# Performance work log

Measured on AMD Instinct MI355X. Metric: run time of the kernel, lower is better.

The kernel has to match this reference:

```python
import jax, jax.numpy as jnp
import numpy as np
import math

B, N, F_IN, F_OUT = 16, 2048, 256, 64


def setup_inputs() -> dict:
    key = jax.random.key(0)
    k1, k2, k3, k4 = jax.random.split(key, 4)
    x = jax.random.normal(k1, (B, N, F_IN), dtype=jnp.float32)
    adj = jax.random.randint(k2, (B, N, N), 0, 2, dtype=jnp.int32)
    stdv = 1.0 / math.sqrt(F_OUT)
    weight = jax.random.uniform(k3, (F_IN, F_OUT), dtype=jnp.float32, minval=-stdv, maxval=stdv)
    # weight2 stdv = 1/sqrt(1) = 1.0
    weight2 = jax.random.uniform(k4, (2 * F_OUT, 1), dtype=jnp.float32, minval=-1.0, maxval=1.0)
    return {"x": x, "adj": adj, "weight": weight, "weight2": weight2}


def reference(x, adj, weight, weight2):
    # h[b,n,o] = (x @ weight)  -- shared linear projection
    h = jnp.einsum("bni,io->bno", x, weight)
    Fo = weight.shape[1]
    # Split additive-attention vector: e_ij = relu(h_i . a_src + h_j . a_dst)
    # Mathematically identical to cat([h_i, h_j]) @ weight2 of the original.
    a_src = weight2[:Fo, 0]
    a_dst = weight2[Fo:, 0]
    s_src = jnp.einsum("bno,o->bn", h, a_src)  # [B, N]
    s_dst = jnp.einsum("bno,o->bn", h, a_dst)  # [B, N]
    e = jax.nn.relu(s_src[:, :, None] + s_dst[:, None, :])  # [B, N, N]
    NEG = jnp.float32(-9e15)
    scores = jnp.where(adj > 0, e, NEG)
    attention = jax.nn.softmax(scores, axis=2)  # softmax over neighbors j
    # dropout = 0.0 / eval mode -> identity
    out = jnp.einsum("bij,bjo->bio", attention, h)  # [B, N, F_OUT]
    return out
```

## Files before the change

kernel.cpp:

```cpp
#include <hip/hip_runtime.h>
#include <hip/hip_bf16.h>

#define BB 16
#define NN 2048
#define FIN 256
#define FO 64

typedef __bf16 bf16x8 __attribute__((ext_vector_type(8)));
typedef float  f32x4  __attribute__((ext_vector_type(4)));
typedef int    i32x4  __attribute__((ext_vector_type(4)));
typedef unsigned int uint;

__global__ __launch_bounds__(256) void k_pack(const int* __restrict__ adj,
                                              unsigned char* __restrict__ mask) {
    size_t t = (size_t)blockIdx.x * 256 + threadIdx.x;
    const i32x4* ap = (const i32x4*)(adj + t * 8);
    i32x4 a0 = __builtin_nontemporal_load(ap);
    i32x4 a1 = __builtin_nontemporal_load(ap + 1);
    unsigned b = (unsigned)(a0.x > 0) | ((unsigned)(a0.y > 0) << 1) |
                 ((unsigned)(a0.z > 0) << 2) | ((unsigned)(a0.w > 0) << 3) |
                 ((unsigned)(a1.x > 0) << 4) | ((unsigned)(a1.y > 0) << 5) |
                 ((unsigned)(a1.z > 0) << 6) | ((unsigned)(a1.w > 0) << 7);
    mask[t] = (unsigned char)b;
}

__global__ __launch_bounds__(256) void k1_gemm(
    const float* __restrict__ x, const float* __restrict__ weight,
    const float* __restrict__ w2,
    __bf16* __restrict__ hT, float* __restrict__ s_src, float* __restrict__ s_dst) {
    __shared__ __bf16 WtL[FO * 264];
    __shared__ float vsL[FIN], vdL[FIN];
    int t = threadIdx.x;
    {
        const float4* wr = (const float4*)(weight + t * FO);
        float a = 0.f, d = 0.f;
#pragma unroll
        for (int c = 0; c < 16; ++c) {
            float4 v = wr[c];
            int o = c * 4;
            WtL[(o + 0) * 264 + t] = (__bf16)v.x;
            WtL[(o + 1) * 264 + t] = (__bf16)v.y;
            WtL[(o + 2) * 264 + t] = (__bf16)v.z;
            WtL[(o + 3) * 264 + t] = (__bf16)v.w;
            a += v.x * w2[o] + v.y * w2[o + 1] + v.z * w2[o + 2] + v.w * w2[o + 3];
            d += v.x * w2[FO + o] + v.y * w2[FO + o + 1] +
                 v.z * w2[FO + o + 2] + v.w * w2[FO + o + 3];
        }
        vsL[t] = a;
        vdL[t] = d;
    }
    __syncthreads();

    int lane = threadIdx.x & 63, w = threadIdx.x >> 6;
    int quad = lane >> 4, m = lane & 15;
    int Rbase = blockIdx.x * 64 + w * 16;
    int R = Rbase + m;
    const float* xr = x + (long)R * FIN;

    f32x4 acc[4] = {};
    float ps = 0.f, pd = 0.f;

#pragma unroll
    for (int k0 = 0; k0 < FIN; k0 += 32) {
        int kb = k0 + quad * 8;
        float4 x0 = *(const float4*)(xr + kb);
        float4 x1 = *(const float4*)(xr + kb + 4);
        float4 u0 = *(const float4*)(vsL + kb);
        float4 u1 = *(const float4*)(vsL + kb + 4);
        float4 t0 = *(const float4*)(vdL + kb);
        float4 t1 = *(const float4*)(vdL + kb + 4);
        ps += x0.x * u0.x + x0.y * u0.y + x0.z * u0.z + x0.w * u0.w +
              x1.x * u1.x + x1.y * u1.y + x1.z * u1.z + x1.w * u1.w;
        pd += x0.x * t0.x + x0.y * t0.y + x0.z * t0.z + x0.w * t0.w +
              x1.x * t1.x + x1.y * t1.y + x1.z * t1.z + x1.w * t1.w;
        bf16x8 bf = {(__bf16)x0.x, (__bf16)x0.y, (__bf16)x0.z, (__bf16)x0.w,
                     (__bf16)x1.x, (__bf16)x1.y, (__bf16)x1.z, (__bf16)x1.w};
#pragma unroll
        for (int ot = 0; ot < 4; ++ot) {
            bf16x8 af = *(const bf16x8*)(WtL + (ot * 16 + m) * 264 + kb);
            acc[ot] = __builtin_amdgcn_mfma_f32_16x16x32_bf16(af, bf, acc[ot], 0, 0, 0);
        }
    }
    ps += __shfl_xor(ps, 16);
    ps += __shfl_xor(ps, 32);
    pd += __shfl_xor(pd, 16);
    pd += __shfl_xor(pd, 32);
    if (quad == 0) {
        s_src[R] = ps;
        s_dst[R] = pd;
    }
    int b = R >> 11;
    int nb = Rbase & (NN - 1);
#pragma unroll
    for (int ot = 0; ot < 4; ++ot) {
#pragma unroll
        for (int r = 0; r < 4; ++r) {
            int o = ot * 16 + quad * 4 + r;
            hT[((long)b * FO + o) * NN + nb + m] = (__bf16)acc[ot][r];
        }
    }
}

__global__ __launch_bounds__(64, 4) void k2_attn(
    const unsigned char* __restrict__ mask, const float* __restrict__ s_src,
    const float* __restrict__ s_dst, const __bf16* __restrict__ hT,
    float* __restrict__ out) {
    __shared__ float EL[NN];
    int b = blockIdx.x >> 7;
    int rowbase = (blockIdx.x & 127) << 4;
    int lane = threadIdx.x & 63;
    int quad = lane >> 4, m = lane & 15;
    int row = rowbase + m;

    const float* sd = s_dst + b * NN;
    float mx = -3.0e38f;
    for (int j = lane; j < NN; j += 64) mx = fmaxf(mx, sd[j]);
#pragma unroll
    for (int off = 32; off >= 1; off >>= 1) mx = fmaxf(mx, __shfl_xor(mx, off));
    for (int t = lane; t < NN; t += 64) EL[t] = __expf(sd[t] - mx);

    float T = s_src[b * NN + row] + mx;
    float cK = __expf(-T);

    const uint4* mrow = (const uint4*)(mask + ((size_t)(b * NN + row)) * 256);
    const __bf16* hTb = hT + (long)b * FO * NN;
    int q8 = quad * 8;

    f32x4 acc[4] = {};
    f32x4 accL = {};
    const bf16x8 ones = {(__bf16)1.f, (__bf16)1.f, (__bf16)1.f, (__bf16)1.f,
                         (__bf16)1.f, (__bf16)1.f, (__bf16)1.f, (__bf16)1.f};

#pragma unroll
    for (int g = 0; g < 4; ++g) {
        uint4 mv0 = mrow[g * 4 + 0];
        uint4 mv1 = mrow[g * 4 + 1];
        uint4 mv2 = mrow[g * 4 + 2];
        uint4 mv3 = mrow[g * 4 + 3];
        uint mg[16] = {mv0.x, mv0.y, mv0.z, mv0.w, mv1.x, mv1.y, mv1.z, mv1.w,
                       mv2.x, mv2.y, mv2.z, mv2.w, mv3.x, mv3.y, mv3.z, mv3.w};
#pragma unroll
        for (int u = 0; u < 16; ++u) {
            int ks = g * 16 + u;
            uint mb = (mg[u] >> q8) & 0xffu;
            const float* ep = EL + ks * 32 + q8;
            float4 e0 = *(const float4*)ep;
            float4 e1 = *(const float4*)(ep + 4);
            float p0 = (mb & 1u)   ? fmaxf(e0.x, cK) : 0.f;
            float p1 = (mb & 2u)   ? fmaxf(e0.y, cK) : 0.f;
            float p2 = (mb & 4u)   ? fmaxf(e0.z, cK) : 0.f;
            float p3 = (mb & 8u)   ? fmaxf(e0.w, cK) : 0.f;
            float p4 = (mb & 16u)  ? fmaxf(e1.x, cK) : 0.f;
            float p5 = (mb & 32u)  ? fmaxf(e1.y, cK) : 0.f;
            float p6 = (mb & 64u)  ? fmaxf(e1.z, cK) : 0.f;
            float p7 = (mb & 128u) ? fmaxf(e1.w, cK) : 0.f;
            bf16x8 af = {(__bf16)p0, (__bf16)p1, (__bf16)p2, (__bf16)p3,
                         (__bf16)p4, (__bf16)p5, (__bf16)p6, (__bf16)p7};
            accL = __builtin_amdgcn_mfma_f32_16x16x32_bf16(af, ones, accL, 0, 0, 0);
            const __bf16* hb = hTb + ks * 32 + q8;
#pragma unroll
            for (int ot = 0; ot < 4; ++ot) {
                bf16x8 bf = *(const bf16x8*)(hb + (ot * 16 + m) * NN);
                acc[ot] = __builtin_amdgcn_mfma_f32_16x16x32_bf16(af, bf, acc[ot], 0, 0, 0);
            }
        }
    }

    float* outp = out + ((long)b * NN + rowbase) * FO;
#pragma unroll
    for (int r = 0; r < 4; ++r) {
        int orow = quad * 4 + r;
        float inv = 1.0f / accL[r];
#pragma unroll
        for (int ot = 0; ot < 4; ++ot) {
            outp[(long)orow * FO + ot * 16 + m] = acc[ot][r] * inv;
        }
    }
}

extern "C" void kernel_launch(void* const* d_in, const int* in_sizes, int n_in,
                              void* d_out, int out_size, void* d_ws, size_t ws_size,
                              hipStream_t stream) {
    const float* x      = (const float*)d_in[0];
    const int*   adj    = (const int*)d_in[1];
    const float* weight = (const float*)d_in[2];
    const float* w2     = (const float*)d_in[3];
    float* out = (float*)d_out;

    char* ws = (char*)d_ws;
    __bf16* hT   = (__bf16*)ws;
    float* s_src = (float*)(ws + 4194304);
    float* s_dst = (float*)(ws + 4194304 + 131072);
    unsigned char* mask = (unsigned char*)(ws + 4194304 + 262144);

    k_pack<<<32768, 256, 0, stream>>>(adj, mask);
    k1_gemm<<<512, 256, 0, stream>>>(x, weight, w2, hT, s_src, s_dst);
    k2_attn<<<2048, 64, 0, stream>>>(mask, s_src, s_dst, hT, out);
}
```

Measured before the change: 439.1 us.

## Stage h chunks in LDS shared by four waves per attention block

```diff
diff --git a/kernel.cpp b/kernel.cpp
--- a/kernel.cpp
+++ b/kernel.cpp
@@ -5,23 +5,29 @@
 #define NN 2048
 #define FIN 256
 #define FO 64
+#define CH 256
+#define HSTR 264
 
 typedef __bf16 bf16x8 __attribute__((ext_vector_type(8)));
 typedef float  f32x4  __attribute__((ext_vector_type(4)));
 typedef int    i32x4  __attribute__((ext_vector_type(4)));
 typedef unsigned int uint;
+typedef unsigned short ushort;
 
 __global__ __launch_bounds__(256) void k_pack(const int* __restrict__ adj,
-                                              unsigned char* __restrict__ mask) {
+                                              ushort* __restrict__ mask) {
     size_t t = (size_t)blockIdx.x * 256 + threadIdx.x;
-    const i32x4* ap = (const i32x4*)(adj + t * 8);
-    i32x4 a0 = __builtin_nontemporal_load(ap);
-    i32x4 a1 = __builtin_nontemporal_load(ap + 1);
-    unsigned b = (unsigned)(a0.x > 0) | ((unsigned)(a0.y > 0) << 1) |
-                 ((unsigned)(a0.z > 0) << 2) | ((unsigned)(a0.w > 0) << 3) |
-                 ((unsigned)(a1.x > 0) << 4) | ((unsigned)(a1.y > 0) << 5) |
-                 ((unsigned)(a1.z > 0) << 6) | ((unsigned)(a1.w > 0) << 7);
-    mask[t] = (unsigned char)b;
+    const i32x4* ap = (const i32x4*)(adj + t * 16);
+    i32x4 a0 = ap[0], a1 = ap[1], a2 = ap[2], a3 = ap[3];
+    uint b = (uint)(a0.x > 0) | ((uint)(a0.y > 0) << 1) |
+             ((uint)(a0.z > 0) << 2) | ((uint)(a0.w > 0) << 3) |
+             ((uint)(a1.x > 0) << 4) | ((uint)(a1.y > 0) << 5) |
+             ((uint)(a1.z > 0) << 6) | ((uint)(a1.w > 0) << 7) |
+             ((uint)(a2.x > 0) << 8) | ((uint)(a2.y > 0) << 9) |
+             ((uint)(a2.z > 0) << 10) | ((uint)(a2.w > 0) << 11) |
+             ((uint)(a3.x > 0) << 12) | ((uint)(a3.y > 0) << 13) |
+             ((uint)(a3.z > 0) << 14) | ((uint)(a3.w > 0) << 15);
+    mask[t] = (ushort)b;
 }
 
 __global__ __launch_bounds__(256) void k1_gemm(
@@ -101,15 +107,17 @@
     }
 }
 
-__global__ __launch_bounds__(64, 4) void k2_attn(
+__global__ __launch_bounds__(256, 4) void k2_attn(
     const unsigned char* __restrict__ mask, const float* __restrict__ s_src,
     const float* __restrict__ s_dst, const __bf16* __restrict__ hT,
     float* __restrict__ out) {
+    __shared__ __bf16 hL[FO * HSTR];
     __shared__ float EL[NN];
-    int b = blockIdx.x >> 7;
-    int rowbase = (blockIdx.x & 127) << 4;
-    int lane = threadIdx.x & 63;
+    int b = blockIdx.x >> 5;
+    int i0 = (blockIdx.x & 31) << 6;
+    int lane = threadIdx.x & 63, w = threadIdx.x >> 6;
     int quad = lane >> 4, m = lane & 15;
+    int rowbase = i0 + w * 16;
     int row = rowbase + m;
 
     const float* sd = s_dst + b * NN;
@@ -117,33 +125,52 @@
     for (int j = lane; j < NN; j += 64) mx = fmaxf(mx, sd[j]);
 #pragma unroll
     for (int off = 32; off >= 1; off >>= 1) mx = fmaxf(mx, __shfl_xor(mx, off));
-    for (int t = lane; t < NN; t += 64) EL[t] = __expf(sd[t] - mx);
+    {
+        int j0 = threadIdx.x * 8;
+        float4 v0 = *(const float4*)(sd + j0);
+        float4 v1 = *(const float4*)(sd + j0 + 4);
+        EL[j0 + 0] = __expf(v0.x - mx);
+        EL[j0 + 1] = __expf(v0.y - mx);
+        EL[j0 + 2] = __expf(v0.z - mx);
+        EL[j0 + 3] = __expf(v0.w - mx);
+        EL[j0 + 4] = __expf(v1.x - mx);
+        EL[j0 + 5] = __expf(v1.y - mx);
+        EL[j0 + 6] = __expf(v1.z - mx);
+        EL[j0 + 7] = __expf(v1.w - mx);
+    }
 
     float T = s_src[b * NN + row] + mx;
     float cK = __expf(-T);
 
     const uint4* mrow = (const uint4*)(mask + ((size_t)(b * NN + row)) * 256);
-    const __bf16* hTb = hT + (long)b * FO * NN;
     int q8 = quad * 8;
+    int so = threadIdx.x >> 2;
+    int sseg = (threadIdx.x & 3) * 64;
 
     f32x4 acc[4] = {};
     f32x4 accL = {};
     const bf16x8 ones = {(__bf16)1.f, (__bf16)1.f, (__bf16)1.f, (__bf16)1.f,
                          (__bf16)1.f, (__bf16)1.f, (__bf16)1.f, (__bf16)1.f};
 
-#pragma unroll
-    for (int g = 0; g < 4; ++g) {
-        uint4 mv0 = mrow[g * 4 + 0];
-        uint4 mv1 = mrow[g * 4 + 1];
-        uint4 mv2 = mrow[g * 4 + 2];
-        uint4 mv3 = mrow[g * 4 + 3];
-        uint mg[16] = {mv0.x, mv0.y, mv0.z, mv0.w, mv1.x, mv1.y, mv1.z, mv1.w,
-                       mv2.x, mv2.y, mv2.z, mv2.w, mv3.x, mv3.y, mv3.z, mv3.w};
-#pragma unroll
-        for (int u = 0; u < 16; ++u) {
-            int ks = g * 16 + u;
+    for (int c = 0; c < NN / CH; ++c) {
+        __syncthreads();
+        {
+            const bf16x8* src =
+                (const bf16x8*)(hT + ((long)b * FO + so) * NN + c * CH + sseg);
+            bf16x8* dst = (bf16x8*)(hL + so * HSTR + sseg);
+            bf16x8 v0 = src[0], v1 = src[1], v2 = src[2], v3 = src[3];
+            bf16x8 v4 = src[4], v5 = src[5], v6 = src[6], v7 = src[7];
+            dst[0] = v0; dst[1] = v1; dst[2] = v2; dst[3] = v3;
+            dst[4] = v4; dst[5] = v5; dst[6] = v6; dst[7] = v7;
+        }
+        __syncthreads();
+        uint4 mv0 = mrow[c * 2], mv1 = mrow[c * 2 + 1];
+        uint mg[8] = {mv0.x, mv0.y, mv0.z, mv0.w, mv1.x, mv1.y, mv1.z, mv1.w};
+#pragma unroll
+        for (int u = 0; u < 8; ++u) {
+            int ksg = c * 8 + u;
             uint mb = (mg[u] >> q8) & 0xffu;
-            const float* ep = EL + ks * 32 + q8;
+            const float* ep = EL + ksg * 32 + q8;
             float4 e0 = *(const float4*)ep;
             float4 e1 = *(const float4*)(ep + 4);
             float p0 = (mb & 1u)   ? fmaxf(e0.x, cK) : 0.f;
@@ -157,10 +184,10 @@
             bf16x8 af = {(__bf16)p0, (__bf16)p1, (__bf16)p2, (__bf16)p3,
                          (__bf16)p4, (__bf16)p5, (__bf16)p6, (__bf16)p7};
             accL = __builtin_amdgcn_mfma_f32_16x16x32_bf16(af, ones, accL, 0, 0, 0);
-            const __bf16* hb = hTb + ks * 32 + q8;
+            const __bf16* hb = hL + u * 32 + q8;
 #pragma unroll
             for (int ot = 0; ot < 4; ++ot) {
-                bf16x8 bf = *(const bf16x8*)(hb + (ot * 16 + m) * NN);
+                bf16x8 bf = *(const bf16x8*)(hb + (ot * 16 + m) * HSTR);
                 acc[ot] = __builtin_amdgcn_mfma_f32_16x16x32_bf16(af, bf, acc[ot], 0, 0, 0);
             }
         }
@@ -193,7 +220,7 @@
     float* s_dst = (float*)(ws + 4194304 + 131072);
     unsigned char* mask = (unsigned char*)(ws + 4194304 + 262144);
 
-    k_pack<<<32768, 256, 0, stream>>>(adj, mask);
+    k_pack<<<16384, 256, 0, stream>>>(adj, (ushort*)mask);
     k1_gemm<<<512, 256, 0, stream>>>(x, weight, w2, hT, s_src, s_dst);
-    k2_attn<<<2048, 64, 0, stream>>>(mask, s_src, s_dst, hT, out);
-}
+    k2_attn<<<512, 256, 0, stream>>>(mask, s_src, s_dst, hT, out);
+}
```

New measurement: 424.0 us. 3.4% less time.
